# Optimization experiments

Hardware: AMD Instinct MI355X
Metric: run time of the kernel (lower is better)

The kernel has to match this reference:

```python
import jax, jax.numpy as jnp
import numpy as np

SEQ_LEN = 96
PRED_LEN = 16
HIDDEN = 64
FEAT = 7
BATCH = 512


def setup_inputs() -> dict:
    key = jax.random.key(0)
    ks = jax.random.split(key, 7)
    s = 1.0 / np.sqrt(HIDDEN)  # PyTorch LSTM/Linear default uniform init bound
    x = jax.random.normal(ks[0], (BATCH, SEQ_LEN, FEAT), jnp.float32)
    W_ih = jax.random.uniform(ks[1], (4 * HIDDEN, FEAT), jnp.float32, -s, s)
    W_hh = jax.random.uniform(ks[2], (4 * HIDDEN, HIDDEN), jnp.float32, -s, s)
    b_ih = jax.random.uniform(ks[3], (4 * HIDDEN,), jnp.float32, -s, s)
    b_hh = jax.random.uniform(ks[4], (4 * HIDDEN,), jnp.float32, -s, s)
    fc_W = jax.random.uniform(ks[5], (FEAT, HIDDEN), jnp.float32, -s, s)
    fc_b = jax.random.uniform(ks[6], (FEAT,), jnp.float32, -s, s)
    return {"x": x, "W_ih": W_ih, "W_hh": W_hh, "b_ih": b_ih, "b_hh": b_hh,
            "fc_W": fc_W, "fc_b": fc_b}


def _lstm_last(x, h, c, W_ih, W_hh, b):
    # Precompute input-to-gate projections for the whole window: [B, T, 4H]
    xg = jnp.einsum('bti,gi->btg', x, W_ih) + b

    def cell(carry, xg_t):
        h, c = carry
        gates = xg_t + h @ W_hh.T            # [B, 4H], PyTorch gate order i,f,g,o
        i, f, g, o = jnp.split(gates, 4, axis=-1)
        i = jax.nn.sigmoid(i)
        f = jax.nn.sigmoid(f)
        g = jnp.tanh(g)
        o = jax.nn.sigmoid(o)
        c = f * c + i * g
        h = o * jnp.tanh(c)
        return (h, c), None

    (h, c), _ = jax.lax.scan(cell, (h, c), jnp.swapaxes(xg, 0, 1))
    return h, c


def reference(x, W_ih, W_hh, b_ih, b_hh, fc_W, fc_b):
    B = x.shape[0]
    b = b_ih + b_hh
    h = jnp.zeros((B, HIDDEN), x.dtype)
    c = jnp.zeros((B, HIDDEN), x.dtype)
    outs = []
    for _ in range(PRED_LEN):
        h, c = _lstm_last(x, h, c, W_ih, W_hh, b)
        pred = h @ fc_W.T + fc_b             # [B, 7]
        outs.append(pred)
        x = jnp.concatenate([x[:, 1:, :], pred[:, None, :]], axis=1)
    return jnp.stack(outs, axis=1)           # [B, PRED_LEN, 7]
```

## Files before the change

kernel.cpp:

```cpp
#include <hip/hip_runtime.h>

#define SEQ_LEN 96
#define PRED_LEN 16
#define HIDDEN 64
#define FEAT 7
#define BATCH 512
#define TL (SEQ_LEN + PRED_LEN)
#define XSTR 8

typedef float v2f __attribute__((ext_vector_type(2)));

#define L2E 1.4426950408889634f

__device__ __forceinline__ float qp_xor1(float v) {
    return __int_as_float(__builtin_amdgcn_mov_dpp(__float_as_int(v), 0xB1, 0xF, 0xF, true));
}

__global__ __launch_bounds__(128)
__attribute__((amdgpu_waves_per_eu(1, 1)))
__attribute__((amdgpu_num_vgpr(256)))
void lstm_ar_kernel(
    const float* __restrict__ x,
    const float* __restrict__ W_ih,
    const float* __restrict__ W_hh,
    const float* __restrict__ b_ih,
    const float* __restrict__ b_hh,
    const float* __restrict__ fc_W,
    const float* __restrict__ fc_b,
    float* __restrict__ out)
{
    __shared__ float xs[TL * XSTR];
    __shared__ float hb0[HIDDEN];
    __shared__ float hb1[HIDDEN];
    __shared__ float fcw[FEAT * HIDDEN];
    __shared__ float fcb[FEAT];

    const int tid = threadIdx.x;
    const int b   = blockIdx.x;
    const int u   = tid >> 1;
    const int s   = tid & 1;

    v2f wh[4][16];
    #pragma unroll
    for (int g = 0; g < 4; ++g) {
        const float* wr = W_hh + (u + (g << 6)) * HIDDEN + (s << 5);
        #pragma unroll
        for (int j = 0; j < 16; ++j) wh[g][j] = *(const v2f*)(wr + 2 * j);
    }
    v2f wx[4][2];
    #pragma unroll
    for (int g = 0; g < 4; ++g)
        #pragma unroll
        for (int i = 0; i < 2; ++i) {
            int c0 = (s << 2) + 2 * i, c1 = c0 + 1;
            wx[g][i].x = W_ih[(u + (g << 6)) * FEAT + c0];
            wx[g][i].y = (c1 < FEAT) ? W_ih[(u + (g << 6)) * FEAT + c1] : 0.0f;
        }
    float bias[4];
    #pragma unroll
    for (int g = 0; g < 4; ++g)
        bias[g] = (s == 0) ? (b_ih[u + (g << 6)] + b_hh[u + (g << 6)]) : 0.0f;

    const float bk  = (s == 1) ? (-2.0f * L2E) : (-L2E);
    const float bm  = (s == 1) ? 2.0f : 1.0f;
    const float bbc = (s == 1) ? -1.0f : 0.0f;

    for (int i = tid; i < TL * XSTR; i += 128) {
        int row = i >> 3, f = i & 7;
        float v = 0.0f;
        if (row < SEQ_LEN && f < FEAT) v = x[b * SEQ_LEN * FEAT + row * FEAT + f];
        xs[i] = v;
    }
    for (int i = tid; i < FEAT * HIDDEN; i += 128) fcw[i] = fc_W[i];
    if (tid < FEAT)   fcb[tid] = fc_b[tid];
    if (tid < HIDDEN) hb0[tid] = 0.0f;
    float c = 0.0f;
    __syncthreads();

    auto step = [&](float4 xv, int nrow,
                    const float* __restrict__ hr, float* __restrict__ hw) -> float4 {
        const float4* h4 = (const float4*)(hr + (s << 5));

        v2f A0, A1, A2, A3;
        A0.x = bias[0]; A0.y = 0.0f;
        A1.x = bias[1]; A1.y = 0.0f;
        A2.x = bias[2]; A2.y = 0.0f;
        A3.x = bias[3]; A3.y = 0.0f;
        v2f xlo; xlo.x = xv.x; xlo.y = xv.y;
        v2f xhi; xhi.x = xv.z; xhi.y = xv.w;
        A0 = __builtin_elementwise_fma(wx[0][0], xlo, A0);
        A1 = __builtin_elementwise_fma(wx[1][0], xlo, A1);
        A2 = __builtin_elementwise_fma(wx[2][0], xlo, A2);
        A3 = __builtin_elementwise_fma(wx[3][0], xlo, A3);
        A0 = __builtin_elementwise_fma(wx[0][1], xhi, A0);
        A1 = __builtin_elementwise_fma(wx[1][1], xhi, A1);
        A2 = __builtin_elementwise_fma(wx[2][1], xhi, A2);
        A3 = __builtin_elementwise_fma(wx[3][1], xhi, A3);

        #pragma unroll
        for (int j = 0; j < 8; ++j) {
            float4 hv = h4[j];
            v2f hlo; hlo.x = hv.x; hlo.y = hv.y;
            v2f hhi; hhi.x = hv.z; hhi.y = hv.w;
            A0 = __builtin_elementwise_fma(wh[0][2*j],   hlo, A0);
            A1 = __builtin_elementwise_fma(wh[1][2*j],   hlo, A1);
            A2 = __builtin_elementwise_fma(wh[2][2*j],   hlo, A2);
            A3 = __builtin_elementwise_fma(wh[3][2*j],   hlo, A3);
            A0 = __builtin_elementwise_fma(wh[0][2*j+1], hhi, A0);
            A1 = __builtin_elementwise_fma(wh[1][2*j+1], hhi, A1);
            A2 = __builtin_elementwise_fma(wh[2][2*j+1], hhi, A2);
            A3 = __builtin_elementwise_fma(wh[3][2*j+1], hhi, A3);
        }

        float r0 = A0.x + A0.y, r1 = A1.x + A1.y;
        float r2 = A2.x + A2.y, r3 = A3.x + A3.y;
        r0 += qp_xor1(r0); r1 += qp_xor1(r1);
        r2 += qp_xor1(r2); r3 += qp_xor1(r3);

        float aa = s ? r0 : r1;
        float ab = s ? r2 : r3;
        float ea = __builtin_amdgcn_exp2f(aa * (-L2E));
        float va = __builtin_amdgcn_rcpf(1.0f + ea);
        float eb = __builtin_amdgcn_exp2f(ab * bk);
        float rb = __builtin_amdgcn_rcpf(1.0f + eb);
        float vb = fmaf(bm, rb, bbc);

        float pa = qp_xor1(va);
        float pb = qp_xor1(vb);
        float gi = s ? va : pa;
        float gf = s ? pa : va;
        float gg = s ? vb : pb;
        float go = s ? pb : vb;

        c = fmaf(gf, c, gi * gg);
        float e2 = __builtin_amdgcn_exp2f(c * (-2.0f * L2E));
        float rr = __builtin_amdgcn_rcpf(1.0f + e2);
        float th = fmaf(2.0f, rr, -1.0f);
        float h  = go * th;

        hw[u] = h;

        float4 nxt = *(const float4*)&xs[nrow * XSTR + (s << 2)];
        __syncthreads();
        return nxt;
    };

    for (int k = 0; k < PRED_LEN; ++k) {
        float4 xv = *(const float4*)&xs[k * XSTR + (s << 2)];
        for (int t = 0; t < SEQ_LEN; t += 2) {
            xv = step(xv, k + t + 1, hb0, hb1);
            xv = step(xv, k + t + 2, hb1, hb0);
        }

        if (tid < FEAT) {
            float p0 = fcb[tid], p1 = 0.0f, p2 = 0.0f, p3 = 0.0f;
            const float4* hh = (const float4*)hb0;
            #pragma unroll
            for (int j = 0; j < 16; ++j) {
                float4 hv = hh[j];
                p0 = fmaf(fcw[tid * HIDDEN + 4*j + 0], hv.x, p0);
                p1 = fmaf(fcw[tid * HIDDEN + 4*j + 1], hv.y, p1);
                p2 = fmaf(fcw[tid * HIDDEN + 4*j + 2], hv.z, p2);
                p3 = fmaf(fcw[tid * HIDDEN + 4*j + 3], hv.w, p3);
            }
            float pred = (p0 + p1) + (p2 + p3);
            out[(b * PRED_LEN + k) * FEAT + tid] = pred;
            xs[(SEQ_LEN + k) * XSTR + tid] = pred;
        }
        __syncthreads();
    }
}

extern "C" void kernel_launch(void* const* d_in, const int* in_sizes, int n_in,
                              void* d_out, int out_size, void* d_ws, size_t ws_size,
                              hipStream_t stream) {
    const float* x    = (const float*)d_in[0];
    const float* W_ih = (const float*)d_in[1];
    const float* W_hh = (const float*)d_in[2];
    const float* b_ih = (const float*)d_in[3];
    const float* b_hh = (const float*)d_in[4];
    const float* fc_W = (const float*)d_in[5];
    const float* fc_b = (const float*)d_in[6];
    float* out = (float*)d_out;

    lstm_ar_kernel<<<BATCH, 128, 0, stream>>>(x, W_ih, W_hh, b_ih, b_hh, fc_W, fc_b, out);
}
```

Measured before the change: 538.9 us.

## Assign one gate row per thread with 256-thread blocks and DPP gate exchange

Restructures the recurrent step so each of 256 threads owns a full W_hh gate row (one of four gates for one hidden unit), instead of 128 threads each holding half-rows for all four gates. Gates are exchanged between the four lanes of a quad with DPP moves, so the cross-lane partial-sum reduction goes away. The bias is folded into the input-projection weights by setting x's padding column to 1. Only lane 0 of each quad writes h; the others write to a scratch buffer to avoid branching. This halves the per-thread FMA chain on the serial critical path, at the cost of twice the threads per block and barrier participants, and drops the 1-wave-per-EU and VGPR attributes.

```diff
diff --git a/kernel.cpp b/kernel.cpp
--- a/kernel.cpp
+++ b/kernel.cpp
@@ -15,10 +15,13 @@
 __device__ __forceinline__ float qp_xor1(float v) {
     return __int_as_float(__builtin_amdgcn_mov_dpp(__float_as_int(v), 0xB1, 0xF, 0xF, true));
 }
+__device__ __forceinline__ float qp_xor2(float v) {
+    return __int_as_float(__builtin_amdgcn_mov_dpp(__float_as_int(v), 0x4E, 0xF, 0xF, true));
+}
 
-__global__ __launch_bounds__(128)
-__attribute__((amdgpu_waves_per_eu(1, 1)))
-__attribute__((amdgpu_num_vgpr(256)))
+struct X2 { float4 a, b; };
+
+__global__ __launch_bounds__(256, 2)
 void lstm_ar_kernel(
     const float* __restrict__ x,
     const float* __restrict__ W_ih,
@@ -32,124 +35,106 @@
     __shared__ float xs[TL * XSTR];
     __shared__ float hb0[HIDDEN];
     __shared__ float hb1[HIDDEN];
+    __shared__ float hscr[64];
     __shared__ float fcw[FEAT * HIDDEN];
     __shared__ float fcb[FEAT];
 
     const int tid = threadIdx.x;
     const int b   = blockIdx.x;
-    const int u   = tid >> 1;
-    const int s   = tid & 1;
+    const int u   = tid >> 2;
+    const int g   = tid & 3;
+    const int row = (g << 6) + u;
 
-    v2f wh[4][16];
+    v2f wh[32];
+    {
+        const float* wr = W_hh + row * HIDDEN;
+        #pragma unroll
+        for (int j = 0; j < 32; ++j) wh[j] = *(const v2f*)(wr + 2 * j);
+    }
+    v2f wx[4];
     #pragma unroll
-    for (int g = 0; g < 4; ++g) {
-        const float* wr = W_hh + (u + (g << 6)) * HIDDEN + (s << 5);
-        #pragma unroll
-        for (int j = 0; j < 16; ++j) wh[g][j] = *(const v2f*)(wr + 2 * j);
+    for (int i = 0; i < 4; ++i) {
+        int c0 = 2 * i, c1 = 2 * i + 1;
+        wx[i].x = W_ih[row * FEAT + c0];
+        wx[i].y = (c1 < FEAT) ? W_ih[row * FEAT + c1]
+                              : (b_ih[row] + b_hh[row]);
     }
-    v2f wx[4][2];
-    #pragma unroll
-    for (int g = 0; g < 4; ++g)
-        #pragma unroll
-        for (int i = 0; i < 2; ++i) {
-            int c0 = (s << 2) + 2 * i, c1 = c0 + 1;
-            wx[g][i].x = W_ih[(u + (g << 6)) * FEAT + c0];
-            wx[g][i].y = (c1 < FEAT) ? W_ih[(u + (g << 6)) * FEAT + c1] : 0.0f;
-        }
-    float bias[4];
-    #pragma unroll
-    for (int g = 0; g < 4; ++g)
-        bias[g] = (s == 0) ? (b_ih[u + (g << 6)] + b_hh[u + (g << 6)]) : 0.0f;
 
-    const float bk  = (s == 1) ? (-2.0f * L2E) : (-L2E);
-    const float bm  = (s == 1) ? 2.0f : 1.0f;
-    const float bbc = (s == 1) ? -1.0f : 0.0f;
+    const float bk  = (g == 2) ? (-2.0f * L2E) : (-L2E);
+    const float bm  = (g == 2) ? 2.0f : 1.0f;
+    const float bbc = (g == 2) ? -1.0f : 0.0f;
 
-    for (int i = tid; i < TL * XSTR; i += 128) {
-        int row = i >> 3, f = i & 7;
-        float v = 0.0f;
-        if (row < SEQ_LEN && f < FEAT) v = x[b * SEQ_LEN * FEAT + row * FEAT + f];
+    float* const wa1 = (g == 0) ? (hb1 + u) : (hscr + (tid & 63));
+    float* const wa0 = (g == 0) ? (hb0 + u) : (hscr + (tid & 63));
+
+    for (int i = tid; i < TL * XSTR; i += 256) {
+        int r = i >> 3, f = i & 7;
+        float v = 1.0f;
+        if (f < FEAT) v = (r < SEQ_LEN) ? x[b * SEQ_LEN * FEAT + r * FEAT + f] : 0.0f;
         xs[i] = v;
     }
-    for (int i = tid; i < FEAT * HIDDEN; i += 128) fcw[i] = fc_W[i];
+    for (int i = tid; i < FEAT * HIDDEN; i += 256) fcw[i] = fc_W[i];
     if (tid < FEAT)   fcb[tid] = fc_b[tid];
     if (tid < HIDDEN) hb0[tid] = 0.0f;
     float c = 0.0f;
     __syncthreads();
 
-    auto step = [&](float4 xv, int nrow,
-                    const float* __restrict__ hr, float* __restrict__ hw) -> float4 {
-        const float4* h4 = (const float4*)(hr + (s << 5));
+    auto step = [&](X2 xv, int nrow, const float* __restrict__ hr,
+                    float* __restrict__ wa) -> X2 {
+        v2f xl0; xl0.x = xv.a.x; xl0.y = xv.a.y;
+        v2f xl1; xl1.x = xv.a.z; xl1.y = xv.a.w;
+        v2f xh0; xh0.x = xv.b.x; xh0.y = xv.b.y;
+        v2f xh1; xh1.x = xv.b.z; xh1.y = xv.b.w;
+        v2f A0 = wx[0] * xl0;
+        v2f A1 = wx[1] * xl1;
+        v2f A2 = wx[2] * xh0;
+        v2f A3 = wx[3] * xh1;
 
-        v2f A0, A1, A2, A3;
-        A0.x = bias[0]; A0.y = 0.0f;
-        A1.x = bias[1]; A1.y = 0.0f;
-        A2.x = bias[2]; A2.y = 0.0f;
-        A3.x = bias[3]; A3.y = 0.0f;
-        v2f xlo; xlo.x = xv.x; xlo.y = xv.y;
-        v2f xhi; xhi.x = xv.z; xhi.y = xv.w;
-        A0 = __builtin_elementwise_fma(wx[0][0], xlo, A0);
-        A1 = __builtin_elementwise_fma(wx[1][0], xlo, A1);
-        A2 = __builtin_elementwise_fma(wx[2][0], xlo, A2);
-        A3 = __builtin_elementwise_fma(wx[3][0], xlo, A3);
-        A0 = __builtin_elementwise_fma(wx[0][1], xhi, A0);
-        A1 = __builtin_elementwise_fma(wx[1][1], xhi, A1);
-        A2 = __builtin_elementwise_fma(wx[2][1], xhi, A2);
-        A3 = __builtin_elementwise_fma(wx[3][1], xhi, A3);
+        const float4* h4 = (const float4*)hr;
+        #pragma unroll
+        for (int j = 0; j < 16; j += 2) {
+            float4 h0 = h4[j];
+            float4 h1 = h4[j + 1];
+            v2f l0; l0.x = h0.x; l0.y = h0.y;
+            v2f i0; i0.x = h0.z; i0.y = h0.w;
+            v2f l1; l1.x = h1.x; l1.y = h1.y;
+            v2f i1; i1.x = h1.z; i1.y = h1.w;
+            A0 = __builtin_elementwise_fma(wh[2 * j],     l0, A0);
+            A1 = __builtin_elementwise_fma(wh[2 * j + 1], i0, A1);
+            A2 = __builtin_elementwise_fma(wh[2 * j + 2], l1, A2);
+            A3 = __builtin_elementwise_fma(wh[2 * j + 3], i1, A3);
+        }
+        A0 = A0 + A2;
+        A1 = A1 + A3;
+        A0 = A0 + A1;
+        float r = A0.x + A0.y;
 
-        #pragma unroll
-        for (int j = 0; j < 8; ++j) {
-            float4 hv = h4[j];
-            v2f hlo; hlo.x = hv.x; hlo.y = hv.y;
-            v2f hhi; hhi.x = hv.z; hhi.y = hv.w;
-            A0 = __builtin_elementwise_fma(wh[0][2*j],   hlo, A0);
-            A1 = __builtin_elementwise_fma(wh[1][2*j],   hlo, A1);
-            A2 = __builtin_elementwise_fma(wh[2][2*j],   hlo, A2);
-            A3 = __builtin_elementwise_fma(wh[3][2*j],   hlo, A3);
-            A0 = __builtin_elementwise_fma(wh[0][2*j+1], hhi, A0);
-            A1 = __builtin_elementwise_fma(wh[1][2*j+1], hhi, A1);
-            A2 = __builtin_elementwise_fma(wh[2][2*j+1], hhi, A2);
-            A3 = __builtin_elementwise_fma(wh[3][2*j+1], hhi, A3);
-        }
+        float e   = __builtin_amdgcn_exp2f(r * bk);
+        float rc  = __builtin_amdgcn_rcpf(1.0f + e);
+        float act = fmaf(bm, rc, bbc);
 
-        float r0 = A0.x + A0.y, r1 = A1.x + A1.y;
-        float r2 = A2.x + A2.y, r3 = A3.x + A3.y;
-        r0 += qp_xor1(r0); r1 += qp_xor1(r1);
-        r2 += qp_xor1(r2); r3 += qp_xor1(r3);
+        float p1 = qp_xor1(act);
+        float p2 = qp_xor2(act);
+        float p3 = qp_xor2(p1);
 
-        float aa = s ? r0 : r1;
-        float ab = s ? r2 : r3;
-        float ea = __builtin_amdgcn_exp2f(aa * (-L2E));
-        float va = __builtin_amdgcn_rcpf(1.0f + ea);
-        float eb = __builtin_amdgcn_exp2f(ab * bk);
-        float rb = __builtin_amdgcn_rcpf(1.0f + eb);
-        float vb = fmaf(bm, rb, bbc);
-
-        float pa = qp_xor1(va);
-        float pb = qp_xor1(vb);
-        float gi = s ? va : pa;
-        float gf = s ? pa : va;
-        float gg = s ? vb : pb;
-        float go = s ? pb : vb;
-
-        c = fmaf(gf, c, gi * gg);
+        c = fmaf(p1, c, act * p2);
         float e2 = __builtin_amdgcn_exp2f(c * (-2.0f * L2E));
         float rr = __builtin_amdgcn_rcpf(1.0f + e2);
         float th = fmaf(2.0f, rr, -1.0f);
-        float h  = go * th;
+        *wa = p3 * th;
 
-        hw[u] = h;
-
-        float4 nxt = *(const float4*)&xs[nrow * XSTR + (s << 2)];
+        const float4* nx = (const float4*)(xs + nrow * XSTR);
+        X2 nxt; nxt.a = nx[0]; nxt.b = nx[1];
         __syncthreads();
         return nxt;
     };
 
     for (int k = 0; k < PRED_LEN; ++k) {
-        float4 xv = *(const float4*)&xs[k * XSTR + (s << 2)];
+        const float4* x0 = (const float4*)(xs + k * XSTR);
+        X2 cur; cur.a = x0[0]; cur.b = x0[1];
         for (int t = 0; t < SEQ_LEN; t += 2) {
-            xv = step(xv, k + t + 1, hb0, hb1);
-            xv = step(xv, k + t + 2, hb1, hb0);
+            cur = step(cur, k + t + 1, hb0, wa1);
+            cur = step(cur, k + t + 2, hb1, wa0);
         }
 
         if (tid < FEAT) {
@@ -158,10 +143,10 @@
             #pragma unroll
             for (int j = 0; j < 16; ++j) {
                 float4 hv = hh[j];
-                p0 = fmaf(fcw[tid * HIDDEN + 4*j + 0], hv.x, p0);
-                p1 = fmaf(fcw[tid * HIDDEN + 4*j + 1], hv.y, p1);
-                p2 = fmaf(fcw[tid * HIDDEN + 4*j + 2], hv.z, p2);
-                p3 = fmaf(fcw[tid * HIDDEN + 4*j + 3], hv.w, p3);
+                p0 = fmaf(fcw[tid * HIDDEN + 4 * j + 0], hv.x, p0);
+                p1 = fmaf(fcw[tid * HIDDEN + 4 * j + 1], hv.y, p1);
+                p2 = fmaf(fcw[tid * HIDDEN + 4 * j + 2], hv.z, p2);
+                p3 = fmaf(fcw[tid * HIDDEN + 4 * j + 3], hv.w, p3);
             }
             float pred = (p0 + p1) + (p2 + p3);
             out[(b * PRED_LEN + k) * FEAT + tid] = pred;
@@ -183,5 +168,5 @@
     const float* fc_b = (const float*)d_in[6];
     float* out = (float*)d_out;
 
-    lstm_ar_kernel<<<BATCH, 128, 0, stream>>>(x, W_ih, W_hh, b_ih, b_hh, fc_W, fc_b, out);
+    lstm_ar_kernel<<<BATCH, 256, 0, stream>>>(x, W_ih, W_hh, b_ih, b_hh, fc_W, fc_b, out);
 }
```

Result: slower. 816.0 us (+51.4%).
